# Kernel optimization log

Hardware: AMD Instinct MI355X
Metric: run time of the kernel (lower is better)

The kernel has to match this reference:

```python
import jax, jax.numpy as jnp
import numpy as np
import math

B, S, DIM, H = 4, 1024, 4096, 32
HD = DIM // H  # head_dim = 128
MAX_B, MAX_S = 4, 1024
START_POS = 0
ROPE_THETA = 10000.0


def setup_inputs() -> dict:
    key = jax.random.key(0)
    ks = jax.random.split(key, 6)
    x = jax.random.normal(ks[0], (B, S, DIM), dtype=jnp.float32)
    # real RoPE frequencies: freqs_cis[t, j] = exp(i * t * theta^{-2j/hd})
    inv_freq = 1.0 / (ROPE_THETA ** (jnp.arange(0, HD, 2, dtype=jnp.float32) / HD))  # [HD/2]
    t = jnp.arange(START_POS, START_POS + S, dtype=jnp.float32)
    ang = jnp.outer(t, inv_freq)  # [S, HD/2]
    freqs_cos = jnp.cos(ang)
    freqs_sin = jnp.sin(ang)
    # additive causal mask as in llama: -inf above diagonal offset start_pos+1
    mask = jnp.triu(jnp.full((1, 1, S, S), float('-inf'), dtype=jnp.float32), k=START_POS + 1)
    scale = 0.02
    wq = jax.random.normal(ks[1], (DIM, DIM), dtype=jnp.float32) * scale
    wk = jax.random.normal(ks[2], (DIM, DIM), dtype=jnp.float32) * scale
    wv = jax.random.normal(ks[3], (DIM, DIM), dtype=jnp.float32) * scale
    wo = jax.random.normal(ks[4], (DIM, DIM), dtype=jnp.float32) * scale
    cache_k = jnp.zeros((MAX_B, MAX_S, H, HD), dtype=jnp.float32)
    cache_v = jnp.zeros((MAX_B, MAX_S, H, HD), dtype=jnp.float32)
    return {"x": x, "start_pos": START_POS, "freqs_cos": freqs_cos, "freqs_sin": freqs_sin,
            "mask": mask, "wq": wq, "wk": wk, "wv": wv, "wo": wo,
            "cache_k": cache_k, "cache_v": cache_v}


def _apply_rotary(t, cos, sin):
    # t: [B, S, H, HD]; interpret last dim as HD/2 complex pairs (real, imag)
    b, s, h, d = t.shape
    tr = t.reshape(b, s, h, d // 2, 2)
    a, bb = tr[..., 0], tr[..., 1]
    c = cos[None, :, None, :]  # [1, S, 1, HD/2]
    si = sin[None, :, None, :]
    out_r = a * c - bb * si
    out_i = a * si + bb * c
    return jnp.stack([out_r, out_i], axis=-1).reshape(b, s, h, d)


def reference(x, start_pos, freqs_cos, freqs_sin, mask, wq, wk, wv, wo, cache_k, cache_v):
    bsz, seqlen, dim = x.shape
    hd = HD
    # torch Linear: y = x @ W.T, W is [out, in]
    xq = (x @ wq.T).reshape(bsz, seqlen, H, hd)
    xk = (x @ wk.T).reshape(bsz, seqlen, H, hd)
    xv = (x @ wv.T).reshape(bsz, seqlen, H, hd)
    xq = _apply_rotary(xq, freqs_cos, freqs_sin)
    xk = _apply_rotary(xk, freqs_cos, freqs_sin)
    # KV-cache write
    cache_k = jax.lax.dynamic_update_slice(cache_k, xk, (0, start_pos, 0, 0))
    cache_v = jax.lax.dynamic_update_slice(cache_v, xv, (0, start_pos, 0, 0))
    keys = cache_k[:bsz, :start_pos + seqlen]    # [B, K, H, HD]
    values = cache_v[:bsz, :start_pos + seqlen]  # [B, K, H, HD]
    # naive attention: full score matrix
    scores = jnp.einsum('bqhd,bkhd->bhqk', xq, keys) / math.sqrt(hd)
    scores = scores + mask
    probs = jax.nn.softmax(scores.astype(jnp.float32), axis=-1).astype(xq.dtype)
    out = jnp.einsum('bhqk,bkhd->bqhd', probs, values)
    out = out.reshape(bsz, seqlen, -1)
    return out @ wo.T
```

## Files before the change

kernel.cpp:

```cpp
#include <hip/hip_runtime.h>
#include <hip/hip_bf16.h>
#include <cstdint>

typedef __hip_bfloat16 bf16;
typedef __attribute__((ext_vector_type(8))) short frag8;
typedef __attribute__((ext_vector_type(4))) float f32x4;

#define DEV __device__ __forceinline__

DEV void gl_lds16(const void* g, void* l) {
  __builtin_amdgcn_global_load_lds(
      (const __attribute__((address_space(1))) void*)g,
      (__attribute__((address_space(3))) void*)l, 16, 0, 0);
}

DEV void storeC(float* C, size_t idx, float v) { C[idx] = v; }
DEV void storeC(bf16* C, size_t idx, float v) { C[idx] = __float2bfloat16(v); }

__global__ __launch_bounds__(256) void conv_kernel(const float* __restrict__ in,
                                                   bf16* __restrict__ out, int n8) {
  int i = blockIdx.x * 256 + threadIdx.x;
  if (i >= n8) return;
  const float4* in4 = reinterpret_cast<const float4*>(in);
  float4 a = in4[2 * i], b = in4[2 * i + 1];
  union { frag8 v; bf16 h[8]; } u;
  u.h[0] = __float2bfloat16(a.x); u.h[1] = __float2bfloat16(a.y);
  u.h[2] = __float2bfloat16(a.z); u.h[3] = __float2bfloat16(a.w);
  u.h[4] = __float2bfloat16(b.x); u.h[5] = __float2bfloat16(b.y);
  u.h[6] = __float2bfloat16(b.z); u.h[7] = __float2bfloat16(b.w);
  *reinterpret_cast<frag8*>(out + (size_t)i * 8) = u.v;
}

#define MF(a, b, c) __builtin_amdgcn_mfma_f32_16x16x32_bf16(a, b, c, 0, 0, 0)

#define STAGE(isB, h, tt, bp) do {                                             \
    char* _d = lds + ((isB) * 65536) + ((((bp) * 2) + (h)) << 14);             \
    gl_lds16(((isB) ? gB : gA)[h][0] + (size_t)(tt) * 64, _d + ldsOff0);       \
    gl_lds16(((isB) ? gB : gA)[h][1] + (size_t)(tt) * 64, _d + ldsOff1);       \
  } while (0)

#define RDA(mi, ckk) (*(const frag8*)(ab + aRowB + (mi) * 2048 + (ckk)))
#define RDB(ni, ckk) (*(const frag8*)(bb + bRowB + (ni) * 2048 + (ckk)))

#define PHASE(p, SSTAGE, SWAIT) do {                                           \
    if ((p) == 0) {                                                            \
      b00 = RDB(0, ck0); b01 = RDB(0, ck1); b10 = RDB(1, ck0); b11 = RDB(1, ck1); \
      b20 = RDB(2, ck0); b21 = RDB(2, ck1); b30 = RDB(3, ck0); b31 = RDB(3, ck1); \
    }                                                                          \
    frag8 a00 = RDA(2 * (p), ck0), a01 = RDA(2 * (p), ck1);                    \
    frag8 a10 = RDA(2 * (p) + 1, ck0), a11 = RDA(2 * (p) + 1, ck1);            \
    SSTAGE;                                                                    \
    SWAIT;                                                                     \
    __builtin_amdgcn_s_barrier();                                              \
    __builtin_amdgcn_s_setprio(1);                                             \
    acc[2*(p)][0]   = MF(a00, b00, acc[2*(p)][0]);                             \
    acc[2*(p)][1]   = MF(a00, b10, acc[2*(p)][1]);                             \
    acc[2*(p)][2]   = MF(a00, b20, acc[2*(p)][2]);                             \
    acc[2*(p)][3]   = MF(a00, b30, acc[2*(p)][3]);                             \
    acc[2*(p)+1][0] = MF(a10, b00, acc[2*(p)+1][0]);                           \
    acc[2*(p)+1][1] = MF(a10, b10, acc[2*(p)+1][1]);                           \
    acc[2*(p)+1][2] = MF(a10, b20, acc[2*(p)+1][2]);                           \
    acc[2*(p)+1][3] = MF(a10, b30, acc[2*(p)+1][3]);                           \
    acc[2*(p)][0]   = MF(a01, b01, acc[2*(p)][0]);                             \
    acc[2*(p)][1]   = MF(a01, b11, acc[2*(p)][1]);                             \
    acc[2*(p)][2]   = MF(a01, b21, acc[2*(p)][2]);                             \
    acc[2*(p)][3]   = MF(a01, b31, acc[2*(p)][3]);                             \
    acc[2*(p)+1][0] = MF(a11, b01, acc[2*(p)+1][0]);                           \
    acc[2*(p)+1][1] = MF(a11, b11, acc[2*(p)+1][1]);                           \
    acc[2*(p)+1][2] = MF(a11, b21, acc[2*(p)+1][2]);                           \
    acc[2*(p)+1][3] = MF(a11, b31, acc[2*(p)+1][3]);                           \
    __builtin_amdgcn_s_setprio(0);                                             \
    __builtin_amdgcn_s_barrier();                                              \
  } while (0)

#define VM4 asm volatile("s_waitcnt vmcnt(4)" ::: "memory")
#define VM0 asm volatile("s_waitcnt vmcnt(0)" ::: "memory")
#define NOW ((void)0)

#define TILE(t, SA, SB, SWAIT) do {                                            \
    const int _bp2 = ((t) & 1) * 2;                                            \
    char* ab = lds + ((_bp2 + wm) << 14);                                      \
    char* bb = lds + 65536 + ((_bp2 + bhalf) << 14);                           \
    PHASE(0, { if (SA) STAGE(0, 0, (t) + 1, ((t) + 1) & 1); }, NOW);           \
    PHASE(1, { if (SA) STAGE(0, 1, (t) + 1, ((t) + 1) & 1); }, NOW);           \
    PHASE(2, { if (SB) STAGE(1, 0, (t) + 2, (t) & 1); }, NOW);                 \
    PHASE(3, { if (SB) STAGE(1, 1, (t) + 2, (t) & 1); }, SWAIT);               \
  } while (0)

template <typename OutT, bool ROPE>
__global__ __launch_bounds__(512, 2) void gemm8(const bf16* __restrict__ A,
                                                const bf16* __restrict__ Bt,
                                                OutT* __restrict__ C,
                                                const float* __restrict__ fc,
                                                const float* __restrict__ fs) {
  __shared__ __align__(16) char lds[131072];
  const int K = 4096, N = 4096;
  const int t = threadIdx.x;
  const int lane = t & 63, w = t >> 6;
  const int wm = w >> 2, wn = w & 3;
  const int lr = lane & 15, lg = lane >> 4;
  const int bhalf = wn >> 1;

  const int bid = blockIdx.x;
  const int wg = (bid & 7) * 32 + (bid >> 3);
  const int m0 = (wg >> 4) * 256, n0 = (wg & 15) * 256;

  const bf16* gA[2][2];
  const bf16* gB[2][2];
  int ldsOff0, ldsOff1;
  {
    int c0 = (w * 2 + 0) * 64 + lane;
    int c1 = (w * 2 + 1) * 64 + lane;
    int r0 = c0 >> 3, r1 = c1 >> 3;
    int e0 = ((c0 & 7) ^ (r0 & 7)) * 8;
    int e1 = ((c1 & 7) ^ (r1 & 7)) * 8;
    ldsOff0 = c0 * 16; ldsOff1 = c1 * 16;
    gA[0][0] = A + (size_t)(m0 + r0) * K + e0;
    gA[0][1] = A + (size_t)(m0 + r1) * K + e1;
    gA[1][0] = A + (size_t)(m0 + 128 + r0) * K + e0;
    gA[1][1] = A + (size_t)(m0 + 128 + r1) * K + e1;
    gB[0][0] = Bt + (size_t)(n0 + r0) * K + e0;
    gB[0][1] = Bt + (size_t)(n0 + r1) * K + e1;
    gB[1][0] = Bt + (size_t)(n0 + 128 + r0) * K + e0;
    gB[1][1] = Bt + (size_t)(n0 + 128 + r1) * K + e1;
  }

  const int swz = (lr & 7) << 4;
  const int ck0 = (lg * 16) ^ swz;
  const int ck1 = (64 + lg * 16) ^ swz;
  const int aRowB = lr * 128;
  const int bRowB = ((wn & 1) * 64 + lr) * 128;

  f32x4 acc[8][4];
#pragma unroll
  for (int mi = 0; mi < 8; ++mi)
#pragma unroll
    for (int ni = 0; ni < 4; ++ni) acc[mi][ni] = (f32x4){0.f, 0.f, 0.f, 0.f};

  frag8 b00, b01, b10, b11, b20, b21, b30, b31;

  STAGE(1, 0, 0, 0); STAGE(1, 1, 0, 0);
  STAGE(0, 0, 0, 0); STAGE(0, 1, 0, 0);
  STAGE(1, 0, 1, 1); STAGE(1, 1, 1, 1);
  VM4;
  __builtin_amdgcn_s_barrier();

  for (int tt = 0; tt < 62; tt += 2) {
    TILE(tt, 1, 1, VM4);
    TILE(tt + 1, 1, 1, VM4);
  }
  TILE(62, 1, 0, VM0);
  TILE(63, 0, 0, NOW);

#pragma unroll
  for (int mi = 0; mi < 8; ++mi)
#pragma unroll
    for (int ni = 0; ni < 4; ++ni) {
      f32x4 v = acc[mi][ni];
      int col = n0 + wn * 64 + ni * 16 + lr;
      if (ROPE) {
        int i = (col & 127) >> 1;
        const bool odd = (col & 1);
#pragma unroll
        for (int ii = 0; ii < 4; ++ii) {
          int row = m0 + wm * 128 + mi * 16 + lg * 4 + ii;
          int s = row & 1023;
          float c = fc[s * 64 + i], si = fs[s * 64 + i];
          float val = v[ii];
          float par = __shfl_xor(val, 1);
          float o = val * c + (odd ? par * si : -par * si);
          storeC(C, (size_t)row * N + col, o);
        }
      } else {
#pragma unroll
        for (int ii = 0; ii < 4; ++ii) {
          int row = m0 + wm * 128 + mi * 16 + lg * 4 + ii;
          storeC(C, (size_t)row * N + col, v[ii]);
        }
      }
    }
}

__global__ __launch_bounds__(256) void transpose_v_kernel(const bf16* __restrict__ v,
                                                          bf16* __restrict__ vt) {
  __shared__ unsigned short tile[32][40];
  const int st = blockIdx.x * 32;
  const int dt = blockIdx.y * 32;
  const int bh = blockIdx.z;
  const int b = bh >> 5, h = bh & 31;
  const int t = threadIdx.x;
  const int r = t >> 3, c4 = (t & 7) * 4;
  const unsigned short* src = reinterpret_cast<const unsigned short*>(v) +
      ((size_t)(b * 1024 + st + r)) * 4096 + h * 128 + dt + c4;
  uint2 d = *reinterpret_cast<const uint2*>(src);
  tile[r][c4 + 0] = (unsigned short)(d.x & 0xffff);
  tile[r][c4 + 1] = (unsigned short)(d.x >> 16);
  tile[r][c4 + 2] = (unsigned short)(d.y & 0xffff);
  tile[r][c4 + 3] = (unsigned short)(d.y >> 16);
  __syncthreads();
  uint2 o;
  o.x = (uint32_t)tile[c4 + 0][r] | ((uint32_t)tile[c4 + 1][r] << 16);
  o.y = (uint32_t)tile[c4 + 2][r] | ((uint32_t)tile[c4 + 3][r] << 16);
  unsigned short* dst = reinterpret_cast<unsigned short*>(vt) +
      ((size_t)bh * 128 + dt + r) * 1024 + st + c4;
  *reinterpret_cast<uint2*>(dst) = o;
}

__global__ __launch_bounds__(512, 4) void attn_kernel(const bf16* __restrict__ q,
                                                      const bf16* __restrict__ k,
                                                      const bf16* __restrict__ vt,
                                                      bf16* __restrict__ out) {
  __shared__ __align__(16) char als[65536];
  const int qt = blockIdx.x, h = blockIdx.y, b = blockIdx.z;
  const int t = threadIdx.x;
  const int lane = t & 63, w = t >> 6;
  const int lr = lane & 15, lg = lane >> 4;
  const int NT = 2 * qt + 2;

  frag8 aq[4];
  {
    const bf16* qp = q + ((size_t)(b * 1024 + qt * 128 + w * 16 + lr)) * 4096 + h * 128 + lg * 8;
#pragma unroll
    for (int ks = 0; ks < 4; ++ks) aq[ks] = *reinterpret_cast<const frag8*>(qp + ks * 32);
  }

  const bf16* kbase = k + (size_t)b * 1024 * 4096 + h * 128;
  const bf16* vbase = vt + ((size_t)(b * 32 + h)) * 128 * 1024;

  const int L0 = t * 16, L1 = (t + 512) * 16;
  const int kr0 = L0 >> 8, kr1 = L1 >> 8;
  const size_t kOff0 = (size_t)kr0 * 4096 + (((L0 & 255) ^ ((kr0 & 7) << 4)) >> 1);
  const size_t kOff1 = (size_t)kr1 * 4096 + (((L1 & 255) ^ ((kr1 & 7) << 4)) >> 1);
  const int vr0 = L0 >> 7, vr1 = L1 >> 7;
  const size_t vOff0 = (size_t)vr0 * 1024 + (((L0 & 127) ^ ((vr0 & 7) << 4)) >> 1);
  const size_t vOff1 = (size_t)vr1 * 1024 + (((L1 & 127) ^ ((vr1 & 7) << 4)) >> 1);

#define STAGE_K(tt, bp) do { char* _d = als + (bp) * 16384;                    \
    gl_lds16(kbase + (size_t)(tt) * 262144 + kOff0, _d + L0);                  \
    gl_lds16(kbase + (size_t)(tt) * 262144 + kOff1, _d + L1); } while (0)
#define STAGE_V(tt, bp) do { char* _d = als + 32768 + (bp) * 16384;            \
    gl_lds16(vbase + (size_t)(tt) * 64 + vOff0, _d + L0);                      \
    gl_lds16(vbase + (size_t)(tt) * 64 + vOff1, _d + L1); } while (0)

  f32x4 oacc[8] = {};
  float mrow = -1e30f, lrow = 0.f;
  const float scale = 0.08838834764831845f;
  const int qmaxw = qt * 128 + w * 16 + 15;
  const int qr_g = qt * 128 + w * 16 + lr;

  STAGE_K(0, 0); STAGE_V(0, 0);
  STAGE_K(1, 1); STAGE_V(1, 1);

  for (int kt = 0; kt < NT; ++kt) {
    const int cur = kt & 1;
    const bool act = (kt * 64 <= qmaxw);
    const bool domask = (kt >= 2 * qt);
    char* Kc = als + cur * 16384;
    char* Vc = als + 32768 + cur * 16384;

    if (kt + 1 < NT) { VM4; } else { VM0; }
    __builtin_amdgcn_s_barrier();

    f32x4 sacc[4] = {};
    if (act) {
      __builtin_amdgcn_s_setprio(1);
#pragma unroll
      for (int ks = 0; ks < 4; ++ks) {
#pragma unroll
        for (int ni = 0; ni < 4; ++ni) {
          int n = ni * 16 + lr;
          frag8 bk = *reinterpret_cast<const frag8*>(
              Kc + n * 256 + ((ks * 64 + lg * 16) ^ ((n & 7) << 4)));
          sacc[ni] = MF(bk, aq[ks], sacc[ni]);
        }
      }
      __builtin_amdgcn_s_setprio(0);
    }
    __builtin_amdgcn_s_barrier();
    if (kt + 2 < NT) STAGE_K(kt + 2, cur);

    if (act) {
#pragma unroll
      for (int ni = 0; ni < 4; ++ni)
#pragma unroll
        for (int i = 0; i < 4; ++i) {
          float x = sacc[ni][i] * scale;
          if (domask) {
            int kc = kt * 64 + ni * 16 + lg * 4 + i;
            if (kc > qr_g) x = -1e30f;
          }
          sacc[ni][i] = x;
        }

      float pm = sacc[0][0];
#pragma unroll
      for (int ni = 0; ni < 4; ++ni)
#pragma unroll
        for (int i = 0; i < 4; ++i) pm = fmaxf(pm, sacc[ni][i]);
      pm = fmaxf(pm, __shfl_xor(pm, 16));
      pm = fmaxf(pm, __shfl_xor(pm, 32));
      float mn = fmaxf(mrow, pm);
      float f = __expf(mrow - mn);
      float rs = 0.f;
#pragma unroll
      for (int ni = 0; ni < 4; ++ni)
#pragma unroll
        for (int i = 0; i < 4; ++i) {
          float p = __expf(sacc[ni][i] - mn);
          sacc[ni][i] = p;
          rs += p;
        }
      rs += __shfl_xor(rs, 16);
      rs += __shfl_xor(rs, 32);
      lrow = lrow * f + rs;
      mrow = mn;

      uint32_t Wrd[8];
#pragma unroll
      for (int ni = 0; ni < 4; ++ni)
#pragma unroll
        for (int jj = 0; jj < 2; ++jj) {
          union { uint32_t u; bf16 hh[2]; } pk;
          pk.hh[0] = __float2bfloat16(sacc[ni][2 * jj]);
          pk.hh[1] = __float2bfloat16(sacc[ni][2 * jj + 1]);
          Wrd[ni * 2 + jj] = pk.u;
        }

      float fi0 = __shfl(f, lg * 4 + 0);
      float fi1 = __shfl(f, lg * 4 + 1);
      float fi2 = __shfl(f, lg * 4 + 2);
      float fi3 = __shfl(f, lg * 4 + 3);
#pragma unroll
      for (int nj = 0; nj < 8; ++nj) {
        oacc[nj][0] *= fi0; oacc[nj][1] *= fi1;
        oacc[nj][2] *= fi2; oacc[nj][3] *= fi3;
      }

      __builtin_amdgcn_s_setprio(1);
#pragma unroll
      for (int ks2 = 0; ks2 < 2; ++ks2) {
        union { frag8 fr; uint32_t w[4]; } apu;
#pragma unroll
        for (int j2 = 0; j2 < 4; ++j2) {
          int src = lr + (((2 * lg) + (j2 >> 1)) & 3) * 16;
          uint32_t lo = __shfl(Wrd[4 * ks2 + (j2 & 1)], src);
          uint32_t hi = __shfl(Wrd[4 * ks2 + 2 + (j2 & 1)], src);
          apu.w[j2] = (lg & 2) ? hi : lo;
        }
#pragma unroll
        for (int nj = 0; nj < 8; ++nj) {
          int d = nj * 16 + lr;
          frag8 bv = *reinterpret_cast<const frag8*>(
              Vc + d * 128 + ((ks2 * 64 + lg * 16) ^ ((d & 7) << 4)));
          oacc[nj] = MF(apu.fr, bv, oacc[nj]);
        }
      }
      __builtin_amdgcn_s_setprio(0);
    }
    __builtin_amdgcn_s_barrier();
    if (kt + 2 < NT) STAGE_V(kt + 2, cur);
  }

  float lv0 = __shfl(lrow, lg * 4 + 0);
  float lv1 = __shfl(lrow, lg * 4 + 1);
  float lv2 = __shfl(lrow, lg * 4 + 2);
  float lv3 = __shfl(lrow, lg * 4 + 3);
#pragma unroll
  for (int nj = 0; nj < 8; ++nj) {
    int srow0 = qt * 128 + w * 16 + lg * 4;
    size_t base = ((size_t)(b * 1024 + srow0)) * 4096 + h * 128 + nj * 16 + lr;
    out[base]          = __float2bfloat16(oacc[nj][0] / lv0);
    out[base + 4096]   = __float2bfloat16(oacc[nj][1] / lv1);
    out[base + 8192]   = __float2bfloat16(oacc[nj][2] / lv2);
    out[base + 12288]  = __float2bfloat16(oacc[nj][3] / lv3);
  }
#undef STAGE_K
#undef STAGE_V
}

extern "C" void kernel_launch(void* const* d_in, const int* in_sizes, int n_in,
                              void* d_out, int out_size, void* d_ws, size_t ws_size,
                              hipStream_t stream) {
  const float* x  = (const float*)d_in[0];
  const float* fc = (const float*)d_in[2];
  const float* fs = (const float*)d_in[3];
  const float* wq = (const float*)d_in[5];
  const float* wk = (const float*)d_in[6];
  const float* wv = (const float*)d_in[7];
  const float* wo = (const float*)d_in[8];
  float* out = (float*)d_out;

  const size_t SZ = (size_t)4096 * 4096 * 2;
  char* w = (char*)d_ws;
  bf16* xb = (bf16*)(w);
  bf16* wb = (bf16*)(w + SZ);
  bf16* qb = (bf16*)(w + 2 * SZ);
  bf16* kb = (bf16*)(w + 3 * SZ);
  bf16* vb = (bf16*)(w + 4 * SZ);
  bf16* vtb = xb;
  bf16* ao  = vb;

  const int n8 = 4096 * 4096 / 8;
  dim3 cgrd(n8 / 256), blk(256);
  dim3 ggrd(256);
  dim3 gblk(512);

  conv_kernel<<<cgrd, blk, 0, stream>>>(x, xb, n8);
  conv_kernel<<<cgrd, blk, 0, stream>>>(wq, wb, n8);
  gemm8<bf16, true><<<ggrd, gblk, 0, stream>>>(xb, wb, qb, fc, fs);
  conv_kernel<<<cgrd, blk, 0, stream>>>(wk, wb, n8);
  gemm8<bf16, true><<<ggrd, gblk, 0, stream>>>(xb, wb, kb, fc, fs);
  conv_kernel<<<cgrd, blk, 0, stream>>>(wv, wb, n8);
  gemm8<bf16, false><<<ggrd, gblk, 0, stream>>>(xb, wb, vb, fc, fs);
  transpose_v_kernel<<<dim3(32, 4, 128), blk, 0, stream>>>(vb, vtb);
  attn_kernel<<<dim3(8, 32, 4), gblk, 0, stream>>>(qb, kb, vtb, ao);
  conv_kernel<<<cgrd, blk, 0, stream>>>(wo, wb, n8);
  gemm8<float, false><<<ggrd, gblk, 0, stream>>>(ao, wb, out, fc, fs);
}
```

Before: 677.3 us.

## Fuse V transpose into GEMM epilogue and stage P through LDS in attention

The V projection GEMM now writes its output directly in transposed [b,h,d,s] layout through a new epilogue, which removes the separate transpose kernel and its round trip through memory. In the attention kernel, the V buffer becomes triple-buffered so K and V for tile kt+2 can be issued together, dropping one barrier per iteration. The softmax probabilities are now written to a per-wave swizzled LDS scratch and read back as MFMA A-fragments, replacing the cross-lane shuffle sequence. The costs are more LDS per block (96KB vs 64KB), which may lower attention occupancy, and strided 8-byte stores in the V GEMM epilogue.

```diff
diff --git a/kernel.cpp b/kernel.cpp
--- a/kernel.cpp
+++ b/kernel.cpp
@@ -87,7 +87,7 @@
     PHASE(3, { if (SB) STAGE(1, 1, (t) + 2, (t) & 1); }, SWAIT);               \
   } while (0)
 
-template <typename OutT, bool ROPE>
+template <typename OutT, int EPI>
 __global__ __launch_bounds__(512, 2) void gemm8(const bf16* __restrict__ A,
                                                 const bf16* __restrict__ Bt,
                                                 OutT* __restrict__ C,
@@ -158,7 +158,7 @@
     for (int ni = 0; ni < 4; ++ni) {
       f32x4 v = acc[mi][ni];
       int col = n0 + wn * 64 + ni * 16 + lr;
-      if (ROPE) {
+      if (EPI == 1) {
         int i = (col & 127) >> 1;
         const bool odd = (col & 1);
 #pragma unroll
@@ -171,6 +171,17 @@
           float o = val * c + (odd ? par * si : -par * si);
           storeC(C, (size_t)row * N + col, o);
         }
+      } else if (EPI == 2) {
+        int row0 = m0 + wm * 128 + mi * 16 + lg * 4;
+        size_t base = ((size_t)(row0 >> 10) * 4096 + col) * 1024 + (row0 & 1023);
+        union { ushort4 s4; unsigned short us[4]; } pk;
+#pragma unroll
+        for (int ii = 0; ii < 4; ++ii) {
+          union { bf16 b; unsigned short u; } cv;
+          cv.b = __float2bfloat16(v[ii]);
+          pk.us[ii] = cv.u;
+        }
+        *reinterpret_cast<ushort4*>(reinterpret_cast<bf16*>(C) + base) = pk.s4;
       } else {
 #pragma unroll
         for (int ii = 0; ii < 4; ++ii) {
@@ -179,38 +190,13 @@
         }
       }
     }
-}
-
-__global__ __launch_bounds__(256) void transpose_v_kernel(const bf16* __restrict__ v,
-                                                          bf16* __restrict__ vt) {
-  __shared__ unsigned short tile[32][40];
-  const int st = blockIdx.x * 32;
-  const int dt = blockIdx.y * 32;
-  const int bh = blockIdx.z;
-  const int b = bh >> 5, h = bh & 31;
-  const int t = threadIdx.x;
-  const int r = t >> 3, c4 = (t & 7) * 4;
-  const unsigned short* src = reinterpret_cast<const unsigned short*>(v) +
-      ((size_t)(b * 1024 + st + r)) * 4096 + h * 128 + dt + c4;
-  uint2 d = *reinterpret_cast<const uint2*>(src);
-  tile[r][c4 + 0] = (unsigned short)(d.x & 0xffff);
-  tile[r][c4 + 1] = (unsigned short)(d.x >> 16);
-  tile[r][c4 + 2] = (unsigned short)(d.y & 0xffff);
-  tile[r][c4 + 3] = (unsigned short)(d.y >> 16);
-  __syncthreads();
-  uint2 o;
-  o.x = (uint32_t)tile[c4 + 0][r] | ((uint32_t)tile[c4 + 1][r] << 16);
-  o.y = (uint32_t)tile[c4 + 2][r] | ((uint32_t)tile[c4 + 3][r] << 16);
-  unsigned short* dst = reinterpret_cast<unsigned short*>(vt) +
-      ((size_t)bh * 128 + dt + r) * 1024 + st + c4;
-  *reinterpret_cast<uint2*>(dst) = o;
 }
 
 __global__ __launch_bounds__(512, 4) void attn_kernel(const bf16* __restrict__ q,
                                                       const bf16* __restrict__ k,
                                                       const bf16* __restrict__ vt,
                                                       bf16* __restrict__ out) {
-  __shared__ __align__(16) char als[65536];
+  __shared__ __align__(16) char als[98304];
   const int qt = blockIdx.x, h = blockIdx.y, b = blockIdx.z;
   const int t = threadIdx.x;
   const int lane = t & 63, w = t >> 6;
@@ -235,28 +221,28 @@
   const size_t vOff0 = (size_t)vr0 * 1024 + (((L0 & 127) ^ ((vr0 & 7) << 4)) >> 1);
   const size_t vOff1 = (size_t)vr1 * 1024 + (((L1 & 127) ^ ((vr1 & 7) << 4)) >> 1);
 
-#define STAGE_K(tt, bp) do { char* _d = als + (bp) * 16384;                    \
+#define STAGE_K(tt) do { char* _d = als + ((tt) & 1) * 16384;                  \
     gl_lds16(kbase + (size_t)(tt) * 262144 + kOff0, _d + L0);                  \
     gl_lds16(kbase + (size_t)(tt) * 262144 + kOff1, _d + L1); } while (0)
-#define STAGE_V(tt, bp) do { char* _d = als + 32768 + (bp) * 16384;            \
+#define STAGE_V(tt) do { char* _d = als + 32768 + ((tt) % 3) * 16384;          \
     gl_lds16(vbase + (size_t)(tt) * 64 + vOff0, _d + L0);                      \
     gl_lds16(vbase + (size_t)(tt) * 64 + vOff1, _d + L1); } while (0)
 
   f32x4 oacc[8] = {};
   float mrow = -1e30f, lrow = 0.f;
+  char* Pw = als + 81920 + w * 2048;
   const float scale = 0.08838834764831845f;
   const int qmaxw = qt * 128 + w * 16 + 15;
   const int qr_g = qt * 128 + w * 16 + lr;
 
-  STAGE_K(0, 0); STAGE_V(0, 0);
-  STAGE_K(1, 1); STAGE_V(1, 1);
+  STAGE_K(0); STAGE_V(0);
+  STAGE_K(1); STAGE_V(1);
 
   for (int kt = 0; kt < NT; ++kt) {
-    const int cur = kt & 1;
     const bool act = (kt * 64 <= qmaxw);
     const bool domask = (kt >= 2 * qt);
-    char* Kc = als + cur * 16384;
-    char* Vc = als + 32768 + cur * 16384;
+    char* Kc = als + (kt & 1) * 16384;
+    char* Vc = als + 32768 + (kt % 3) * 16384;
 
     if (kt + 1 < NT) { VM4; } else { VM0; }
     __builtin_amdgcn_s_barrier();
@@ -277,7 +263,7 @@
       __builtin_amdgcn_s_setprio(0);
     }
     __builtin_amdgcn_s_barrier();
-    if (kt + 2 < NT) STAGE_K(kt + 2, cur);
+    if (kt + 2 < NT) { STAGE_K(kt + 2); STAGE_V(kt + 2); }
 
     if (act) {
 #pragma unroll
@@ -315,7 +301,6 @@
       lrow = lrow * f + rs;
       mrow = mn;
 
-      uint32_t Wrd[8];
 #pragma unroll
       for (int ni = 0; ni < 4; ++ni)
 #pragma unroll
@@ -323,7 +308,8 @@
           union { uint32_t u; bf16 hh[2]; } pk;
           pk.hh[0] = __float2bfloat16(sacc[ni][2 * jj]);
           pk.hh[1] = __float2bfloat16(sacc[ni][2 * jj + 1]);
-          Wrd[ni * 2 + jj] = pk.u;
+          int kc2 = (ni * 16 + lg * 4 + 2 * jj) * 2;
+          *reinterpret_cast<uint32_t*>(Pw + lr * 128 + (kc2 ^ ((lr & 7) << 4))) = pk.u;
         }
 
       float fi0 = __shfl(f, lg * 4 + 0);
@@ -339,26 +325,18 @@
       __builtin_amdgcn_s_setprio(1);
 #pragma unroll
       for (int ks2 = 0; ks2 < 2; ++ks2) {
-        union { frag8 fr; uint32_t w[4]; } apu;
-#pragma unroll
-        for (int j2 = 0; j2 < 4; ++j2) {
-          int src = lr + (((2 * lg) + (j2 >> 1)) & 3) * 16;
-          uint32_t lo = __shfl(Wrd[4 * ks2 + (j2 & 1)], src);
-          uint32_t hi = __shfl(Wrd[4 * ks2 + 2 + (j2 & 1)], src);
-          apu.w[j2] = (lg & 2) ? hi : lo;
-        }
+        frag8 ap = *reinterpret_cast<const frag8*>(
+            Pw + lr * 128 + ((ks2 * 64 + lg * 16) ^ ((lr & 7) << 4)));
 #pragma unroll
         for (int nj = 0; nj < 8; ++nj) {
           int d = nj * 16 + lr;
           frag8 bv = *reinterpret_cast<const frag8*>(
               Vc + d * 128 + ((ks2 * 64 + lg * 16) ^ ((d & 7) << 4)));
-          oacc[nj] = MF(apu.fr, bv, oacc[nj]);
+          oacc[nj] = MF(ap, bv, oacc[nj]);
         }
       }
       __builtin_amdgcn_s_setprio(0);
     }
-    __builtin_amdgcn_s_barrier();
-    if (kt + 2 < NT) STAGE_V(kt + 2, cur);
   }
 
   float lv0 = __shfl(lrow, lg * 4 + 0);
@@ -392,13 +370,12 @@
 
   const size_t SZ = (size_t)4096 * 4096 * 2;
   char* w = (char*)d_ws;
-  bf16* xb = (bf16*)(w);
-  bf16* wb = (bf16*)(w + SZ);
-  bf16* qb = (bf16*)(w + 2 * SZ);
-  bf16* kb = (bf16*)(w + 3 * SZ);
-  bf16* vb = (bf16*)(w + 4 * SZ);
-  bf16* vtb = xb;
-  bf16* ao  = vb;
+  bf16* xb  = (bf16*)(w);
+  bf16* wb  = (bf16*)(w + SZ);
+  bf16* qb  = (bf16*)(w + 2 * SZ);
+  bf16* kb  = (bf16*)(w + 3 * SZ);
+  bf16* vtb = (bf16*)(w + 4 * SZ);
+  bf16* ao  = xb;
 
   const int n8 = 4096 * 4096 / 8;
   dim3 cgrd(n8 / 256), blk(256);
@@ -407,13 +384,12 @@
 
   conv_kernel<<<cgrd, blk, 0, stream>>>(x, xb, n8);
   conv_kernel<<<cgrd, blk, 0, stream>>>(wq, wb, n8);
-  gemm8<bf16, true><<<ggrd, gblk, 0, stream>>>(xb, wb, qb, fc, fs);
+  gemm8<bf16, 1><<<ggrd, gblk, 0, stream>>>(xb, wb, qb, fc, fs);
   conv_kernel<<<cgrd, blk, 0, stream>>>(wk, wb, n8);
-  gemm8<bf16, true><<<ggrd, gblk, 0, stream>>>(xb, wb, kb, fc, fs);
+  gemm8<bf16, 1><<<ggrd, gblk, 0, stream>>>(xb, wb, kb, fc, fs);
   conv_kernel<<<cgrd, blk, 0, stream>>>(wv, wb, n8);
-  gemm8<bf16, false><<<ggrd, gblk, 0, stream>>>(xb, wb, vb, fc, fs);
-  transpose_v_kernel<<<dim3(32, 4, 128), blk, 0, stream>>>(vb, vtb);
+  gemm8<bf16, 2><<<ggrd, gblk, 0, stream>>>(xb, wb, vtb, fc, fs);
   attn_kernel<<<dim3(8, 32, 4), gblk, 0, stream>>>(qb, kb, vtb, ao);
   conv_kernel<<<cgrd, blk, 0, stream>>>(wo, wb, n8);
-  gemm8<float, false><<<ggrd, gblk, 0, stream>>>(ao, wb, out, fc, fs);
-}
+  gemm8<float, 0><<<ggrd, gblk, 0, stream>>>(ao, wb, out, fc, fs);
+}
```

Result: slower. 694.6 us (+2.6%).
